# Optimization experiments

Hardware: AMD Instinct MI355X
Metric: run time of the kernel (lower is better)

The kernel has to match this reference:

```python
import jax, jax.numpy as jnp
import numpy as np

N_NODES = 20000
N_INPUT = 64
K_MAX = 12
BITS = 64
N_OUT = 10
BATCH = 64
T = 128


def setup_inputs() -> dict:
    key = jax.random.key(0)
    ks = jax.random.split(key, 8)
    x = jax.random.randint(ks[0], (BATCH, T, BITS), 0, 2, dtype=jnp.int32)
    w_in = jax.random.randint(ks[1], (BITS, N_INPUT), 0, 2, dtype=jnp.int32)
    adj_list = jax.random.randint(ks[2], (N_NODES, K_MAX), 0, N_NODES, dtype=jnp.int32)
    adj_mask = jax.random.randint(ks[3], (N_NODES, K_MAX), 0, 2, dtype=jnp.int32)
    lut = jax.random.randint(ks[4], (N_NODES, 2 ** K_MAX), 0, 2, dtype=jnp.int32)
    init_states = jax.random.randint(ks[5], (1, N_NODES), 0, 2, dtype=jnp.int32)
    W_out = jax.random.normal(ks[6], (N_OUT, N_NODES - N_INPUT), dtype=jnp.float32) * 0.02
    b_out = jnp.zeros((N_OUT,), dtype=jnp.float32)
    return {"x": x, "w_in": w_in, "adj_list": adj_list, "adj_mask": adj_mask,
            "lut": lut, "init_states": init_states, "W_out": W_out, "b_out": b_out}


def reference(x, w_in, adj_list, adj_mask, lut, init_states, W_out, b_out):
    B, T_, bits = x.shape
    N, k = adj_list.shape
    I = w_in.shape[1]
    # powers_of_2, big-endian order as in make_minimal_powers_of_two (flip)
    powers = (2 ** jnp.arange(k - 1, -1, -1)).astype(jnp.int32)  # [k]
    no_neigh = ~(adj_mask.astype(bool).any(axis=1))              # [N] nodes w/o neighbours keep state
    node_ids = jnp.arange(N)
    states0 = jnp.broadcast_to(init_states, (B, N)).astype(jnp.int32)

    def step(states, x_t):
        # inject input: bipartite mapping of input bits onto first I nodes (OR-combine)
        u = ((x_t @ w_in) > 0).astype(jnp.int32)                 # [B, I]
        states = states.at[:, :I].set(u)
        # gather incoming neighbour states per node (irregular gather)
        neigh = jnp.take(states, adj_list, axis=1)               # [B, N, k]
        neigh = neigh * adj_mask[None, :, :]
        # bit-pack into LUT index
        idx = (neigh * powers[None, None, :]).sum(axis=-1)       # [B, N], < 2^k
        new = lut[node_ids[None, :], idx]                        # [B, N] LUT lookup
        new = jnp.where(no_neigh[None, :], states, new)
        return new, None

    states, _ = jax.lax.scan(step, states0, jnp.swapaxes(x, 0, 1))
    # readout on reservoir (non-input) nodes at final timestep
    feats = states[:, I:].astype(jnp.float32)                    # [B, N-I]
    out = jax.nn.sigmoid(feats @ W_out.T + b_out)                # [B, n_outputs]
    return out
```

## Files before the change

kernel.cpp:

```cpp
#include <hip/hip_runtime.h>
#include <cstdint>
#include <cstddef>


#define N_NODES   20000
#define N_INPUT   64
#define K_MAX     12
#define T_STEPS   128
#define N_BATCH   64
#define N_OUT     10
#define N_FEAT    (N_NODES - N_INPUT)
#define DUMMY_NODE 20000
#define ST_WORDS  20004

#define NBLK 512
#define NTHR 512
#define NPB  39
#define NPB_PAD 40
#define BAR_CNT 64
#define GO_CNT  8
#define BAR_STRIDE 32

typedef unsigned long long u64;

__global__ __launch_bounds__(256) void pack_x_kernel(const int* __restrict__ x,
                                                     u64* __restrict__ xp) {
  const int t = blockIdx.x;
  const int wave = threadIdx.x >> 6, lane = threadIdx.x & 63;
  for (int b = wave; b < N_BATCH; b += 4) {
    int v = x[((size_t)b * T_STEPS + t) * 64 + lane];
    u64 bal = __ballot(v != 0);
    if (lane == 0) xp[(size_t)t * N_BATCH + b] = bal;
  }
}

__global__ __launch_bounds__(256) void init_kernel(const int* __restrict__ inis,
                                                   const int* __restrict__ w_in,
                                                   const u64* __restrict__ xp,
                                                   u64* __restrict__ buf0,
                                                   u64* __restrict__ buf1,
                                                   u64* __restrict__ wcol,
                                                   unsigned* __restrict__ bar) {
  if (blockIdx.x < 79) {
    int n = blockIdx.x * 256 + threadIdx.x;
    if (n >= N_INPUT && n < ST_WORDS) {
      u64 w = (n < N_NODES && inis[n] != 0) ? ~0ull : 0ull;
      buf0[n] = w;
      buf1[n] = w;
    }
  } else {
    const int wave = threadIdx.x >> 6, lane = threadIdx.x & 63;
    u64 xw = xp[lane];
    for (int i = wave; i < 64; i += 4) {
      int wv = w_in[(size_t)lane * 64 + i];
      u64 wc = __ballot(wv != 0);
      if (lane == 0) wcol[i] = wc;
      u64 ub = __ballot((xw & wc) != 0);
      if (lane == 0) buf0[i] = ub;
    }
    if (threadIdx.x < BAR_CNT + GO_CNT)
      bar[threadIdx.x * BAR_STRIDE] = 0u;
  }
}

__global__ __launch_bounds__(64) void u_pre_kernel(const u64* __restrict__ xp,
                                                   const u64* __restrict__ wcol,
                                                   u64* __restrict__ u_all) {
  const int t = blockIdx.x, lane = threadIdx.x;
  u64 xw = xp[(size_t)t * N_BATCH + lane];
  for (int i = 0; i < 64; i++) {
    u64 ub = __ballot((xw & wcol[i]) != 0);
    if (lane == 0) u_all[(size_t)t * 64 + i] = ub;
  }
}

__device__ __forceinline__ u64 bit_transpose64(u64 w, int lane) {
  const u64 LO0 = 0x00000000FFFFFFFFull, LO1 = 0x0000FFFF0000FFFFull,
            LO2 = 0x00FF00FF00FF00FFull, LO3 = 0x0F0F0F0F0F0F0F0Full,
            LO4 = 0x3333333333333333ull, LO5 = 0x5555555555555555ull;
#define XP_STAGE(d, LO)                                                  \
  {                                                                      \
    u64 p = (u64)__shfl_xor((long long)w, (d), 64);                      \
    if (lane & (d)) w = ((p >> (d)) & (LO)) | (w & ~(LO));               \
    else            w = (w & (LO)) | ((p << (d)) & ~(LO));               \
  }
  XP_STAGE(32, LO0) XP_STAGE(16, LO1) XP_STAGE(8, LO2)
  XP_STAGE(4,  LO3) XP_STAGE(2,  LO4) XP_STAGE(1, LO5)
#undef XP_STAGE
  return w;
}

__global__ __launch_bounds__(NTHR, 4) void reservoir_kernel(
    const int* __restrict__ lut, const int* __restrict__ adj,
    const int* __restrict__ mask, const u64* __restrict__ u_all,
    u64* __restrict__ buf0, u64* __restrict__ buf1,
    unsigned* __restrict__ bar) {
  __shared__ u64 lut_lds[NPB_PAD * 64];
  __shared__ int adj_lds[NPB_PAD * K_MAX];
  __shared__ unsigned char hn_lds[NPB_PAD];

  const int bi = blockIdx.x;
  const int tid = threadIdx.x;
  const int wave = tid >> 6, lane = tid & 63;
  const int base = N_INPUT + bi * NPB;
  const int nloc = min(NPB, N_NODES - base);

  if (tid < NPB_PAD) {
    int i = tid, h = 0;
    if (i < nloc) {
      for (int j = 0; j < K_MAX; j++) {
        int m = mask[(size_t)(base + i) * K_MAX + j];
        int a = adj[(size_t)(base + i) * K_MAX + j];
        adj_lds[i * K_MAX + (K_MAX - 1 - j)] = m ? a : DUMMY_NODE;
        h |= m;
      }
    } else {
      for (int j = 0; j < K_MAX; j++) adj_lds[i * K_MAX + j] = DUMMY_NODE;
    }
    hn_lds[i] = (unsigned char)(h ? 1 : 0);
  }

  const int nwords = nloc * 64;
  const int* lp = lut + (size_t)base * 4096;
  for (int w0 = wave * 8; w0 < nwords; w0 += 64) {
    int v[8];
#pragma unroll
    for (int q = 0; q < 8; q++) {
      int widx = w0 + q;
      v[q] = (widx < nwords) ? lp[(size_t)widx * 64 + lane] : 0;
    }
#pragma unroll
    for (int q = 0; q < 8; q++) {
      int widx = w0 + q;
      u64 bal = __ballot(v[q] != 0);
      if (lane == 0 && widx < nwords) lut_lds[widx] = bal;
    }
  }
  __syncthreads();

  const int l0 = wave * 5;
  const int cnt = min(5, nloc - l0);

  int my_a = DUMMY_NODE;
  if (lane < 60) my_a = adj_lds[l0 * K_MAX + lane];
  unsigned hmask = 0;
#pragma unroll
  for (int i = 0; i < 5; i++) hmask |= (unsigned)hn_lds[l0 + i] << i;

  for (int t = 0; t < T_STEPS; t++) {
    u64* cur = (t & 1) ? buf1 : buf0;
    u64* nxt = (t & 1) ? buf0 : buf1;

    u64 w = __hip_atomic_load(&cur[my_a], __ATOMIC_RELAXED,
                              __HIP_MEMORY_SCOPE_AGENT);
    w = bit_transpose64(w, lane);

#pragma unroll
    for (int i = 0; i < 5; i++) {
      if (i < cnt) {
        unsigned idx = (unsigned)(w >> (12 * i)) & 0xFFFu;
        u64 g = lut_lds[(l0 + i) * 64 + (idx >> 6)];
        u64 res = __ballot((g >> (idx & 63)) & 1ull);
        if (lane == 0 && ((hmask >> i) & 1u))
          __hip_atomic_store(&nxt[base + l0 + i], res,
                             __ATOMIC_RELAXED, __HIP_MEMORY_SCOPE_AGENT);
      }
    }

    if (bi == NBLK - 1 && wave == 7 && t + 1 < T_STEPS) {
      u64 uw = u_all[(size_t)(t + 1) * 64 + lane];
      __hip_atomic_store(&nxt[lane], uw, __ATOMIC_RELAXED, __HIP_MEMORY_SCOPE_AGENT);
    }

    if (t != T_STEPS - 1) {
      __syncthreads();
      __builtin_amdgcn_fence(__ATOMIC_RELEASE, "workgroup");
      if (tid == 0)
        __hip_atomic_fetch_add(&bar[(bi & (BAR_CNT - 1)) * BAR_STRIDE], 1u,
                               __ATOMIC_RELAXED, __HIP_MEMORY_SCOPE_AGENT);
      if (bi == 0 && wave == 0) {
        const unsigned tgt = (unsigned)(t + 1) * (NBLK / BAR_CNT);
        for (;;) {
          unsigned c = __hip_atomic_load(&bar[lane * BAR_STRIDE],
                                         __ATOMIC_RELAXED, __HIP_MEMORY_SCOPE_AGENT);
          if (__all(c >= tgt)) break;
        }
        if (lane < GO_CNT)
          __hip_atomic_store(&bar[(BAR_CNT + lane) * BAR_STRIDE], (unsigned)(t + 1),
                             __ATOMIC_RELAXED, __HIP_MEMORY_SCOPE_AGENT);
      } else if (wave == 0) {
        unsigned* gp = &bar[(BAR_CNT + (bi & (GO_CNT - 1))) * BAR_STRIDE];
        while (__hip_atomic_load(gp, __ATOMIC_RELAXED, __HIP_MEMORY_SCOPE_AGENT)
               < (unsigned)(t + 1)) {  }
      }
      __builtin_amdgcn_fence(__ATOMIC_ACQUIRE, "workgroup");
      __syncthreads();
    }
  }
}

__global__ __launch_bounds__(256) void readout_kernel(const u64* __restrict__ st,
                                                      const float* __restrict__ Wout,
                                                      const float* __restrict__ bout,
                                                      float* __restrict__ out) {
  const int b = blockIdx.x / N_OUT;
  const int o = blockIdx.x % N_OUT;
  float acc = 0.f;
  for (int n = threadIdx.x; n < N_FEAT; n += 256) {
    u64 s = st[N_INPUT + n];
    float w = Wout[(size_t)o * N_FEAT + n];
    acc += ((s >> b) & 1ull) ? w : 0.f;
  }
  for (int off = 32; off > 0; off >>= 1) acc += __shfl_down(acc, off);
  __shared__ float red[4];
  const int wave = threadIdx.x >> 6, lane = threadIdx.x & 63;
  if (lane == 0) red[wave] = acc;
  __syncthreads();
  if (threadIdx.x == 0) {
    float tot = red[0] + red[1] + red[2] + red[3] + bout[o];
    out[(size_t)b * N_OUT + o] = 1.f / (1.f + __expf(-tot));
  }
}

extern "C" void kernel_launch(void* const* d_in, const int* in_sizes, int n_in,
                              void* d_out, int out_size, void* d_ws, size_t ws_size,
                              hipStream_t stream) {
  const int* x    = (const int*)d_in[0];
  const int* w_in = (const int*)d_in[1];
  const int* adj  = (const int*)d_in[2];
  const int* mask = (const int*)d_in[3];
  const int* lut  = (const int*)d_in[4];
  const int* inis = (const int*)d_in[5];
  const float* Wout = (const float*)d_in[6];
  const float* bout = (const float*)d_in[7];
  float* out = (float*)d_out;

  char* ws = (char*)d_ws;
  size_t off = 0;
  auto alloc = [&](size_t bytes) -> void* {
    void* p = ws + off;
    off += (bytes + 255) & ~(size_t)255;
    return p;
  };
  u64* buf0 = (u64*)alloc((size_t)ST_WORDS * 8);
  u64* buf1 = (u64*)alloc((size_t)ST_WORDS * 8);
  u64* xp   = (u64*)alloc((size_t)T_STEPS * N_BATCH * 8);
  u64* wcol = (u64*)alloc(64 * 8);
  u64* u_all = (u64*)alloc((size_t)T_STEPS * 64 * 8);
  unsigned* bar = (unsigned*)alloc((size_t)(BAR_CNT + GO_CNT) * BAR_STRIDE * 4);
  (void)ws_size; (void)in_sizes; (void)n_in; (void)out_size;

  hipLaunchKernelGGL(pack_x_kernel, dim3(T_STEPS), dim3(256), 0, stream, x, xp);
  hipLaunchKernelGGL(init_kernel, dim3(80), dim3(256), 0, stream,
                     inis, w_in, xp, buf0, buf1, wcol, bar);
  hipLaunchKernelGGL(u_pre_kernel, dim3(T_STEPS), dim3(64), 0, stream,
                     xp, wcol, u_all);

  hipLaunchKernelGGL(reservoir_kernel, dim3(NBLK), dim3(NTHR), 0, stream,
                     lut, adj, mask, u_all, buf0, buf1, bar);

  hipLaunchKernelGGL(readout_kernel, dim3(N_BATCH * N_OUT), dim3(256), 0, stream,
                     buf0, Wout, bout, out);
}
```

Before: 963.8 us.

## Shrink persistent grid to 128 blocks, prepack LUT, flatten grid barrier

Reduces the persistent reservoir grid from 512 to 128 workgroups of 1024 threads, with each wave now handling 10 nodes through two gathers and transposes. This cuts the number of participants in the per-timestep grid barrier. The barrier drops the atomic fetch-add counters in favour of per-block flag stores, which block 0 scans with 64-bit loads, and the pollers keep a second load in flight. LUT bit-packing moves into a separate full-grid kernel, so the persistent kernel only copies pre-packed words into LDS. The trade-off is fewer blocks for latency hiding and an extra pass over the 328 MB LUT, though that pass is fully parallel.

```diff
diff --git a/kernel.cpp b/kernel.cpp
--- a/kernel.cpp
+++ b/kernel.cpp
@@ -13,13 +13,16 @@
 #define DUMMY_NODE 20000
 #define ST_WORDS  20004
 
-#define NBLK 512
-#define NTHR 512
-#define NPB  39
-#define NPB_PAD 40
-#define BAR_CNT 64
+#define NBLK 128
+#define NTHR 1024
+#define NWAVE 16
+#define NPW  10
+#define NPB  156
+#define NPB_PAD 160
+#define GO_OFF  256
 #define GO_CNT  8
-#define BAR_STRIDE 32
+#define GO_STRIDE 32
+#define PL_BLK 2500
 
 typedef unsigned long long u64;
 
@@ -31,6 +34,17 @@
     int v = x[((size_t)b * T_STEPS + t) * 64 + lane];
     u64 bal = __ballot(v != 0);
     if (lane == 0) xp[(size_t)t * N_BATCH + b] = bal;
+  }
+}
+
+__global__ __launch_bounds__(512) void pack_lut_kernel(const int* __restrict__ lut,
+                                                       u64* __restrict__ lutp) {
+  const int wave = threadIdx.x >> 6, lane = threadIdx.x & 63;
+  const int nwords = N_NODES * 64;
+  for (int widx = blockIdx.x * 8 + wave; widx < nwords; widx += PL_BLK * 8) {
+    int v = lut[(size_t)widx * 64 + lane];
+    u64 bal = __ballot(v != 0);
+    if (lane == 0) lutp[widx] = bal;
   }
 }
 
@@ -58,8 +72,10 @@
       u64 ub = __ballot((xw & wc) != 0);
       if (lane == 0) buf0[i] = ub;
     }
-    if (threadIdx.x < BAR_CNT + GO_CNT)
-      bar[threadIdx.x * BAR_STRIDE] = 0u;
+    if (threadIdx.x < NBLK)
+      bar[threadIdx.x] = 0u;
+    else if (threadIdx.x < NBLK + GO_CNT)
+      bar[GO_OFF + (threadIdx.x - NBLK) * GO_STRIDE] = 0u;
   }
 }
 
@@ -91,7 +107,7 @@
 }
 
 __global__ __launch_bounds__(NTHR, 4) void reservoir_kernel(
-    const int* __restrict__ lut, const int* __restrict__ adj,
+    const u64* __restrict__ lutp, const int* __restrict__ adj,
     const int* __restrict__ mask, const u64* __restrict__ u_all,
     u64* __restrict__ buf0, u64* __restrict__ buf1,
     unsigned* __restrict__ bar) {
@@ -120,45 +136,37 @@
     hn_lds[i] = (unsigned char)(h ? 1 : 0);
   }
 
+  const u64* lp = lutp + (size_t)base * 64;
   const int nwords = nloc * 64;
-  const int* lp = lut + (size_t)base * 4096;
-  for (int w0 = wave * 8; w0 < nwords; w0 += 64) {
-    int v[8];
-#pragma unroll
-    for (int q = 0; q < 8; q++) {
-      int widx = w0 + q;
-      v[q] = (widx < nwords) ? lp[(size_t)widx * 64 + lane] : 0;
-    }
-#pragma unroll
-    for (int q = 0; q < 8; q++) {
-      int widx = w0 + q;
-      u64 bal = __ballot(v[q] != 0);
-      if (lane == 0 && widx < nwords) lut_lds[widx] = bal;
-    }
-  }
+  for (int idx = tid; idx < nwords; idx += NTHR)
+    lut_lds[idx] = lp[idx];
   __syncthreads();
 
-  const int l0 = wave * 5;
-  const int cnt = min(5, nloc - l0);
-
-  int my_a = DUMMY_NODE;
-  if (lane < 60) my_a = adj_lds[l0 * K_MAX + lane];
+  const int l0 = wave * NPW;
+  const int cnt = min(NPW, nloc - l0);
+
+  int a0 = DUMMY_NODE, a1 = DUMMY_NODE;
+  if (lane < 60) {
+    a0 = adj_lds[l0 * K_MAX + lane];
+    a1 = adj_lds[(l0 + 5) * K_MAX + lane];
+  }
   unsigned hmask = 0;
 #pragma unroll
-  for (int i = 0; i < 5; i++) hmask |= (unsigned)hn_lds[l0 + i] << i;
+  for (int i = 0; i < NPW; i++) hmask |= (unsigned)hn_lds[l0 + i] << i;
 
   for (int t = 0; t < T_STEPS; t++) {
     u64* cur = (t & 1) ? buf1 : buf0;
     u64* nxt = (t & 1) ? buf0 : buf1;
 
-    u64 w = __hip_atomic_load(&cur[my_a], __ATOMIC_RELAXED,
-                              __HIP_MEMORY_SCOPE_AGENT);
-    w = bit_transpose64(w, lane);
+    u64 w0 = __hip_atomic_load(&cur[a0], __ATOMIC_RELAXED, __HIP_MEMORY_SCOPE_AGENT);
+    u64 w1 = __hip_atomic_load(&cur[a1], __ATOMIC_RELAXED, __HIP_MEMORY_SCOPE_AGENT);
+    w0 = bit_transpose64(w0, lane);
+    w1 = bit_transpose64(w1, lane);
 
 #pragma unroll
     for (int i = 0; i < 5; i++) {
       if (i < cnt) {
-        unsigned idx = (unsigned)(w >> (12 * i)) & 0xFFFu;
+        unsigned idx = (unsigned)(w0 >> (12 * i)) & 0xFFFu;
         u64 g = lut_lds[(l0 + i) * 64 + (idx >> 6)];
         u64 res = __ballot((g >> (idx & 63)) & 1ull);
         if (lane == 0 && ((hmask >> i) & 1u))
@@ -166,32 +174,50 @@
                              __ATOMIC_RELAXED, __HIP_MEMORY_SCOPE_AGENT);
       }
     }
-
-    if (bi == NBLK - 1 && wave == 7 && t + 1 < T_STEPS) {
+#pragma unroll
+    for (int i = 0; i < 5; i++) {
+      if (i + 5 < cnt) {
+        unsigned idx = (unsigned)(w1 >> (12 * i)) & 0xFFFu;
+        u64 g = lut_lds[(l0 + 5 + i) * 64 + (idx >> 6)];
+        u64 res = __ballot((g >> (idx & 63)) & 1ull);
+        if (lane == 0 && ((hmask >> (i + 5)) & 1u))
+          __hip_atomic_store(&nxt[base + l0 + 5 + i], res,
+                             __ATOMIC_RELAXED, __HIP_MEMORY_SCOPE_AGENT);
+      }
+    }
+
+    if (bi == NBLK - 1 && wave == NWAVE - 1 && t + 1 < T_STEPS) {
       u64 uw = u_all[(size_t)(t + 1) * 64 + lane];
       __hip_atomic_store(&nxt[lane], uw, __ATOMIC_RELAXED, __HIP_MEMORY_SCOPE_AGENT);
     }
 
     if (t != T_STEPS - 1) {
+      const unsigned tgt = (unsigned)(t + 1);
       __syncthreads();
       __builtin_amdgcn_fence(__ATOMIC_RELEASE, "workgroup");
       if (tid == 0)
-        __hip_atomic_fetch_add(&bar[(bi & (BAR_CNT - 1)) * BAR_STRIDE], 1u,
-                               __ATOMIC_RELAXED, __HIP_MEMORY_SCOPE_AGENT);
+        __hip_atomic_store(&bar[bi], tgt, __ATOMIC_RELAXED, __HIP_MEMORY_SCOPE_AGENT);
       if (bi == 0 && wave == 0) {
-        const unsigned tgt = (unsigned)(t + 1) * (NBLK / BAR_CNT);
+        const u64* fp = (const u64*)bar;
+        u64 fa = __hip_atomic_load(&fp[lane], __ATOMIC_RELAXED, __HIP_MEMORY_SCOPE_AGENT);
+        u64 fb = __hip_atomic_load(&fp[lane], __ATOMIC_RELAXED, __HIP_MEMORY_SCOPE_AGENT);
         for (;;) {
-          unsigned c = __hip_atomic_load(&bar[lane * BAR_STRIDE],
-                                         __ATOMIC_RELAXED, __HIP_MEMORY_SCOPE_AGENT);
-          if (__all(c >= tgt)) break;
+          bool ok = ((unsigned)fa >= tgt) && ((unsigned)(fa >> 32) >= tgt);
+          if (__all(ok)) break;
+          fa = fb;
+          fb = __hip_atomic_load(&fp[lane], __ATOMIC_RELAXED, __HIP_MEMORY_SCOPE_AGENT);
         }
         if (lane < GO_CNT)
-          __hip_atomic_store(&bar[(BAR_CNT + lane) * BAR_STRIDE], (unsigned)(t + 1),
+          __hip_atomic_store(&bar[GO_OFF + lane * GO_STRIDE], tgt,
                              __ATOMIC_RELAXED, __HIP_MEMORY_SCOPE_AGENT);
       } else if (wave == 0) {
-        unsigned* gp = &bar[(BAR_CNT + (bi & (GO_CNT - 1))) * BAR_STRIDE];
-        while (__hip_atomic_load(gp, __ATOMIC_RELAXED, __HIP_MEMORY_SCOPE_AGENT)
-               < (unsigned)(t + 1)) {  }
+        unsigned* gp = &bar[GO_OFF + (bi & (GO_CNT - 1)) * GO_STRIDE];
+        unsigned ga = __hip_atomic_load(gp, __ATOMIC_RELAXED, __HIP_MEMORY_SCOPE_AGENT);
+        unsigned gb = __hip_atomic_load(gp, __ATOMIC_RELAXED, __HIP_MEMORY_SCOPE_AGENT);
+        while (ga < tgt) {
+          ga = gb;
+          gb = __hip_atomic_load(gp, __ATOMIC_RELAXED, __HIP_MEMORY_SCOPE_AGENT);
+        }
       }
       __builtin_amdgcn_fence(__ATOMIC_ACQUIRE, "workgroup");
       __syncthreads();
@@ -247,17 +273,19 @@
   u64* xp   = (u64*)alloc((size_t)T_STEPS * N_BATCH * 8);
   u64* wcol = (u64*)alloc(64 * 8);
   u64* u_all = (u64*)alloc((size_t)T_STEPS * 64 * 8);
-  unsigned* bar = (unsigned*)alloc((size_t)(BAR_CNT + GO_CNT) * BAR_STRIDE * 4);
+  unsigned* bar = (unsigned*)alloc((size_t)(GO_OFF + GO_CNT * GO_STRIDE) * 4);
+  u64* lutp = (u64*)alloc((size_t)N_NODES * 64 * 8);
   (void)ws_size; (void)in_sizes; (void)n_in; (void)out_size;
 
   hipLaunchKernelGGL(pack_x_kernel, dim3(T_STEPS), dim3(256), 0, stream, x, xp);
+  hipLaunchKernelGGL(pack_lut_kernel, dim3(PL_BLK), dim3(512), 0, stream, lut, lutp);
   hipLaunchKernelGGL(init_kernel, dim3(80), dim3(256), 0, stream,
                      inis, w_in, xp, buf0, buf1, wcol, bar);
   hipLaunchKernelGGL(u_pre_kernel, dim3(T_STEPS), dim3(64), 0, stream,
                      xp, wcol, u_all);
 
   hipLaunchKernelGGL(reservoir_kernel, dim3(NBLK), dim3(NTHR), 0, stream,
-                     lut, adj, mask, u_all, buf0, buf1, bar);
+                     lutp, adj, mask, u_all, buf0, buf1, bar);
 
   hipLaunchKernelGGL(readout_kernel, dim3(N_BATCH * N_OUT), dim3(256), 0, stream,
                      buf0, Wout, bout, out);
```

Measured after the change: 1.097 ms. +13.8%, slower.

## Replace centralized grid barrier with per-step state buffers and flag polling

Applied to the files above, without the earlier changes.

Keeps a separate state buffer for every timestep, so writes never race with reads of older states. The centralized counter-and-go barrier is replaced by per-block step flags, replicated four ways, which one watcher wave per block polls before releasing the other waves through LDS. Input injection is precomputed straight into each step's buffer, and LUT bit-packing moves into a separate grid-wide pre-kernel instead of running inside each persistent block. The cost is a larger workspace (129 state copies plus the packed LUT), filling every buffer with the initial state, and spin-waiting on LDS.

```diff
diff --git a/kernel.cpp b/kernel.cpp
--- a/kernel.cpp
+++ b/kernel.cpp
@@ -12,14 +12,18 @@
 #define N_FEAT    (N_NODES - N_INPUT)
 #define DUMMY_NODE 20000
 #define ST_WORDS  20004
+#define T_BUF     (T_STEPS + 1)
 
 #define NBLK 512
 #define NTHR 512
 #define NPB  39
 #define NPB_PAD 40
-#define BAR_CNT 64
-#define GO_CNT  8
-#define BAR_STRIDE 32
+#define WATCH_WAVE 7
+#define FL_REP 4
+#define FL_STRIDE 1024
+#define PL_FILL 39
+#define PL_LUT  2500
+#define PL_TOT  (PL_FILL + PL_LUT)
 
 typedef unsigned long long u64;
 
@@ -34,43 +38,52 @@
   }
 }
 
-__global__ __launch_bounds__(256) void init_kernel(const int* __restrict__ inis,
-                                                   const int* __restrict__ w_in,
-                                                   const u64* __restrict__ xp,
-                                                   u64* __restrict__ buf0,
-                                                   u64* __restrict__ buf1,
-                                                   u64* __restrict__ wcol,
-                                                   unsigned* __restrict__ bar) {
-  if (blockIdx.x < 79) {
-    int n = blockIdx.x * 256 + threadIdx.x;
-    if (n >= N_INPUT && n < ST_WORDS) {
+__global__ __launch_bounds__(512) void pack_lut_fill_kernel(
+    const int* __restrict__ lut, const int* __restrict__ inis,
+    u64* __restrict__ lutp, u64* __restrict__ st_all) {
+  if (blockIdx.x < PL_FILL) {
+    int n = N_INPUT + blockIdx.x * 512 + threadIdx.x;
+    if (n < ST_WORDS) {
       u64 w = (n < N_NODES && inis[n] != 0) ? ~0ull : 0ull;
-      buf0[n] = w;
-      buf1[n] = w;
+      for (int t = 0; t < T_BUF; t++)
+        st_all[(size_t)t * ST_WORDS + n] = w;
     }
   } else {
     const int wave = threadIdx.x >> 6, lane = threadIdx.x & 63;
-    u64 xw = xp[lane];
+    const int nwords = N_NODES * 64;
+    for (int widx = (blockIdx.x - PL_FILL) * 8 + wave; widx < nwords;
+         widx += PL_LUT * 8) {
+      int v = lut[(size_t)widx * 64 + lane];
+      u64 bal = __ballot(v != 0);
+      if (lane == 0) lutp[widx] = bal;
+    }
+  }
+}
+
+__global__ __launch_bounds__(256) void init_kernel(const int* __restrict__ w_in,
+                                                   u64* __restrict__ wcol,
+                                                   unsigned* __restrict__ fl) {
+  if (blockIdx.x == 0) {
+    const int wave = threadIdx.x >> 6, lane = threadIdx.x & 63;
     for (int i = wave; i < 64; i += 4) {
       int wv = w_in[(size_t)lane * 64 + i];
       u64 wc = __ballot(wv != 0);
       if (lane == 0) wcol[i] = wc;
-      u64 ub = __ballot((xw & wc) != 0);
-      if (lane == 0) buf0[i] = ub;
-    }
-    if (threadIdx.x < BAR_CNT + GO_CNT)
-      bar[threadIdx.x * BAR_STRIDE] = 0u;
+    }
+  } else {
+    for (int k = threadIdx.x; k < FL_REP * FL_STRIDE; k += 256)
+      fl[k] = 0u;
   }
 }
 
 __global__ __launch_bounds__(64) void u_pre_kernel(const u64* __restrict__ xp,
                                                    const u64* __restrict__ wcol,
-                                                   u64* __restrict__ u_all) {
+                                                   u64* __restrict__ st_all) {
   const int t = blockIdx.x, lane = threadIdx.x;
   u64 xw = xp[(size_t)t * N_BATCH + lane];
   for (int i = 0; i < 64; i++) {
     u64 ub = __ballot((xw & wcol[i]) != 0);
-    if (lane == 0) u_all[(size_t)t * 64 + i] = ub;
+    if (lane == 0) st_all[(size_t)t * ST_WORDS + i] = ub;
   }
 }
 
@@ -91,19 +104,21 @@
 }
 
 __global__ __launch_bounds__(NTHR, 4) void reservoir_kernel(
-    const int* __restrict__ lut, const int* __restrict__ adj,
-    const int* __restrict__ mask, const u64* __restrict__ u_all,
-    u64* __restrict__ buf0, u64* __restrict__ buf1,
-    unsigned* __restrict__ bar) {
+    const u64* __restrict__ lutp, const int* __restrict__ adj,
+    const int* __restrict__ mask, u64* __restrict__ st_all,
+    unsigned* __restrict__ fl) {
   __shared__ u64 lut_lds[NPB_PAD * 64];
   __shared__ int adj_lds[NPB_PAD * K_MAX];
   __shared__ unsigned char hn_lds[NPB_PAD];
+  __shared__ int avail_lds;
 
   const int bi = blockIdx.x;
   const int tid = threadIdx.x;
   const int wave = tid >> 6, lane = tid & 63;
   const int base = N_INPUT + bi * NPB;
   const int nloc = min(NPB, N_NODES - base);
+
+  if (tid == 0) avail_lds = 0;
 
   if (tid < NPB_PAD) {
     int i = tid, h = 0;
@@ -120,39 +135,51 @@
     hn_lds[i] = (unsigned char)(h ? 1 : 0);
   }
 
+  const u64* lp = lutp + (size_t)base * 64;
   const int nwords = nloc * 64;
-  const int* lp = lut + (size_t)base * 4096;
-  for (int w0 = wave * 8; w0 < nwords; w0 += 64) {
-    int v[8];
-#pragma unroll
-    for (int q = 0; q < 8; q++) {
-      int widx = w0 + q;
-      v[q] = (widx < nwords) ? lp[(size_t)widx * 64 + lane] : 0;
-    }
-#pragma unroll
-    for (int q = 0; q < 8; q++) {
-      int widx = w0 + q;
-      u64 bal = __ballot(v[q] != 0);
-      if (lane == 0 && widx < nwords) lut_lds[widx] = bal;
-    }
-  }
+  for (int idx = tid; idx < nwords; idx += NTHR)
+    lut_lds[idx] = lp[idx];
   __syncthreads();
 
   const int l0 = wave * 5;
   const int cnt = min(5, nloc - l0);
 
-  int my_a = DUMMY_NODE;
-  if (lane < 60) my_a = adj_lds[l0 * K_MAX + lane];
+  int a0 = DUMMY_NODE;
+  if (lane < 60) a0 = adj_lds[l0 * K_MAX + lane];
   unsigned hmask = 0;
 #pragma unroll
   for (int i = 0; i < 5; i++) hmask |= (unsigned)hn_lds[l0 + i] << i;
 
+  const u64* fp = (const u64*)(fl + (size_t)(bi & (FL_REP - 1)) * FL_STRIDE);
+
   for (int t = 0; t < T_STEPS; t++) {
-    u64* cur = (t & 1) ? buf1 : buf0;
-    u64* nxt = (t & 1) ? buf0 : buf1;
-
-    u64 w = __hip_atomic_load(&cur[my_a], __ATOMIC_RELAXED,
-                              __HIP_MEMORY_SCOPE_AGENT);
+    if (t) {
+      if (wave == WATCH_WAVE) {
+        const unsigned tgt = (unsigned)t;
+        for (;;) {
+          u64 f0 = __hip_atomic_load(&fp[lane],       __ATOMIC_RELAXED, __HIP_MEMORY_SCOPE_AGENT);
+          u64 f1 = __hip_atomic_load(&fp[64 + lane],  __ATOMIC_RELAXED, __HIP_MEMORY_SCOPE_AGENT);
+          u64 f2 = __hip_atomic_load(&fp[128 + lane], __ATOMIC_RELAXED, __HIP_MEMORY_SCOPE_AGENT);
+          u64 f3 = __hip_atomic_load(&fp[192 + lane], __ATOMIC_RELAXED, __HIP_MEMORY_SCOPE_AGENT);
+          bool ok = (unsigned)f0 >= tgt && (unsigned)(f0 >> 32) >= tgt &&
+                    (unsigned)f1 >= tgt && (unsigned)(f1 >> 32) >= tgt &&
+                    (unsigned)f2 >= tgt && (unsigned)(f2 >> 32) >= tgt &&
+                    (unsigned)f3 >= tgt && (unsigned)(f3 >> 32) >= tgt;
+          if (__all(ok)) break;
+        }
+        __builtin_amdgcn_fence(__ATOMIC_ACQUIRE, "workgroup");
+        if (lane == 0)
+          __hip_atomic_store(&avail_lds, t, __ATOMIC_RELAXED, __HIP_MEMORY_SCOPE_WORKGROUP);
+      } else {
+        while (__hip_atomic_load(&avail_lds, __ATOMIC_RELAXED, __HIP_MEMORY_SCOPE_WORKGROUP) < t) {}
+        __builtin_amdgcn_fence(__ATOMIC_ACQUIRE, "workgroup");
+      }
+    }
+
+    const u64* stc = st_all + (size_t)t * ST_WORDS;
+    u64* stn = st_all + (size_t)(t + 1) * ST_WORDS;
+
+    u64 w = __hip_atomic_load(&stc[a0], __ATOMIC_RELAXED, __HIP_MEMORY_SCOPE_AGENT);
     w = bit_transpose64(w, lane);
 
 #pragma unroll
@@ -162,39 +189,17 @@
         u64 g = lut_lds[(l0 + i) * 64 + (idx >> 6)];
         u64 res = __ballot((g >> (idx & 63)) & 1ull);
         if (lane == 0 && ((hmask >> i) & 1u))
-          __hip_atomic_store(&nxt[base + l0 + i], res,
+          __hip_atomic_store(&stn[base + l0 + i], res,
                              __ATOMIC_RELAXED, __HIP_MEMORY_SCOPE_AGENT);
       }
-    }
-
-    if (bi == NBLK - 1 && wave == 7 && t + 1 < T_STEPS) {
-      u64 uw = u_all[(size_t)(t + 1) * 64 + lane];
-      __hip_atomic_store(&nxt[lane], uw, __ATOMIC_RELAXED, __HIP_MEMORY_SCOPE_AGENT);
     }
 
     if (t != T_STEPS - 1) {
       __syncthreads();
       __builtin_amdgcn_fence(__ATOMIC_RELEASE, "workgroup");
-      if (tid == 0)
-        __hip_atomic_fetch_add(&bar[(bi & (BAR_CNT - 1)) * BAR_STRIDE], 1u,
-                               __ATOMIC_RELAXED, __HIP_MEMORY_SCOPE_AGENT);
-      if (bi == 0 && wave == 0) {
-        const unsigned tgt = (unsigned)(t + 1) * (NBLK / BAR_CNT);
-        for (;;) {
-          unsigned c = __hip_atomic_load(&bar[lane * BAR_STRIDE],
-                                         __ATOMIC_RELAXED, __HIP_MEMORY_SCOPE_AGENT);
-          if (__all(c >= tgt)) break;
-        }
-        if (lane < GO_CNT)
-          __hip_atomic_store(&bar[(BAR_CNT + lane) * BAR_STRIDE], (unsigned)(t + 1),
-                             __ATOMIC_RELAXED, __HIP_MEMORY_SCOPE_AGENT);
-      } else if (wave == 0) {
-        unsigned* gp = &bar[(BAR_CNT + (bi & (GO_CNT - 1))) * BAR_STRIDE];
-        while (__hip_atomic_load(gp, __ATOMIC_RELAXED, __HIP_MEMORY_SCOPE_AGENT)
-               < (unsigned)(t + 1)) {  }
-      }
-      __builtin_amdgcn_fence(__ATOMIC_ACQUIRE, "workgroup");
-      __syncthreads();
+      if (tid < FL_REP)
+        __hip_atomic_store(&fl[tid * FL_STRIDE + bi], (unsigned)(t + 1),
+                           __ATOMIC_RELAXED, __HIP_MEMORY_SCOPE_AGENT);
     }
   }
 }
@@ -242,23 +247,23 @@
     off += (bytes + 255) & ~(size_t)255;
     return p;
   };
-  u64* buf0 = (u64*)alloc((size_t)ST_WORDS * 8);
-  u64* buf1 = (u64*)alloc((size_t)ST_WORDS * 8);
-  u64* xp   = (u64*)alloc((size_t)T_STEPS * N_BATCH * 8);
-  u64* wcol = (u64*)alloc(64 * 8);
-  u64* u_all = (u64*)alloc((size_t)T_STEPS * 64 * 8);
-  unsigned* bar = (unsigned*)alloc((size_t)(BAR_CNT + GO_CNT) * BAR_STRIDE * 4);
+  u64* st_all = (u64*)alloc((size_t)T_BUF * ST_WORDS * 8);
+  u64* xp     = (u64*)alloc((size_t)T_STEPS * N_BATCH * 8);
+  u64* wcol   = (u64*)alloc(64 * 8);
+  unsigned* fl = (unsigned*)alloc((size_t)FL_REP * FL_STRIDE * 4);
+  u64* lutp   = (u64*)alloc((size_t)N_NODES * 64 * 8);
   (void)ws_size; (void)in_sizes; (void)n_in; (void)out_size;
 
   hipLaunchKernelGGL(pack_x_kernel, dim3(T_STEPS), dim3(256), 0, stream, x, xp);
-  hipLaunchKernelGGL(init_kernel, dim3(80), dim3(256), 0, stream,
-                     inis, w_in, xp, buf0, buf1, wcol, bar);
+  hipLaunchKernelGGL(pack_lut_fill_kernel, dim3(PL_TOT), dim3(512), 0, stream,
+                     lut, inis, lutp, st_all);
+  hipLaunchKernelGGL(init_kernel, dim3(2), dim3(256), 0, stream, w_in, wcol, fl);
   hipLaunchKernelGGL(u_pre_kernel, dim3(T_STEPS), dim3(64), 0, stream,
-                     xp, wcol, u_all);
+                     xp, wcol, st_all);
 
   hipLaunchKernelGGL(reservoir_kernel, dim3(NBLK), dim3(NTHR), 0, stream,
-                     lut, adj, mask, u_all, buf0, buf1, bar);
+                     lutp, adj, mask, st_all, fl);
 
   hipLaunchKernelGGL(readout_kernel, dim3(N_BATCH * N_OUT), dim3(256), 0, stream,
-                     buf0, Wout, bout, out);
-}
+                     st_all + (size_t)T_STEPS * ST_WORDS, Wout, bout, out);
+}
```

Result: slower. 1.208 ms (+25.4%).

## Replace atomic-counter grid barrier with per-block flags and split readout

Applied to the files above, without the earlier changes.

The grid barrier no longer has blocks fetch-add into 64 shared counters. Each block now stores the step number into its own flag word, and block 0 polls all 512 flags with packed 64-bit loads before releasing the go flags. This is meant to remove atomic RMW contention on the barrier counters at every timestep. The readout also changes: each thread now handles one batch bit across a chunk of features, partial sums go to a buffer, and a second tiny kernel reduces them and applies the sigmoid. The aim is to cut redundant reads of the state and W_out, at the cost of one extra kernel launch.

```diff
diff --git a/kernel.cpp b/kernel.cpp
--- a/kernel.cpp
+++ b/kernel.cpp
@@ -17,9 +17,13 @@
 #define NTHR 512
 #define NPB  39
 #define NPB_PAD 40
-#define BAR_CNT 64
+#define GO_OFF  512
 #define GO_CNT  8
-#define BAR_STRIDE 32
+#define GO_STRIDE 32
+#define FL_TOT  (GO_OFF + GO_CNT * GO_STRIDE)
+
+#define RO_CHUNK 32
+#define RO_NPC   623
 
 typedef unsigned long long u64;
 
@@ -40,7 +44,7 @@
                                                    u64* __restrict__ buf0,
                                                    u64* __restrict__ buf1,
                                                    u64* __restrict__ wcol,
-                                                   unsigned* __restrict__ bar) {
+                                                   unsigned* __restrict__ fl) {
   if (blockIdx.x < 79) {
     int n = blockIdx.x * 256 + threadIdx.x;
     if (n >= N_INPUT && n < ST_WORDS) {
@@ -58,8 +62,8 @@
       u64 ub = __ballot((xw & wc) != 0);
       if (lane == 0) buf0[i] = ub;
     }
-    if (threadIdx.x < BAR_CNT + GO_CNT)
-      bar[threadIdx.x * BAR_STRIDE] = 0u;
+    for (int k = threadIdx.x; k < FL_TOT; k += 256)
+      fl[k] = 0u;
   }
 }
 
@@ -94,7 +98,7 @@
     const int* __restrict__ lut, const int* __restrict__ adj,
     const int* __restrict__ mask, const u64* __restrict__ u_all,
     u64* __restrict__ buf0, u64* __restrict__ buf1,
-    unsigned* __restrict__ bar) {
+    unsigned* __restrict__ fl) {
   __shared__ u64 lut_lds[NPB_PAD * 64];
   __shared__ int adj_lds[NPB_PAD * K_MAX];
   __shared__ unsigned char hn_lds[NPB_PAD];
@@ -141,8 +145,8 @@
   const int l0 = wave * 5;
   const int cnt = min(5, nloc - l0);
 
-  int my_a = DUMMY_NODE;
-  if (lane < 60) my_a = adj_lds[l0 * K_MAX + lane];
+  int a0 = DUMMY_NODE;
+  if (lane < 60) a0 = adj_lds[l0 * K_MAX + lane];
   unsigned hmask = 0;
 #pragma unroll
   for (int i = 0; i < 5; i++) hmask |= (unsigned)hn_lds[l0 + i] << i;
@@ -151,8 +155,7 @@
     u64* cur = (t & 1) ? buf1 : buf0;
     u64* nxt = (t & 1) ? buf0 : buf1;
 
-    u64 w = __hip_atomic_load(&cur[my_a], __ATOMIC_RELAXED,
-                              __HIP_MEMORY_SCOPE_AGENT);
+    u64 w = __hip_atomic_load(&cur[a0], __ATOMIC_RELAXED, __HIP_MEMORY_SCOPE_AGENT);
     w = bit_transpose64(w, lane);
 
 #pragma unroll
@@ -173,25 +176,29 @@
     }
 
     if (t != T_STEPS - 1) {
+      const unsigned tgt = (unsigned)(t + 1);
       __syncthreads();
       __builtin_amdgcn_fence(__ATOMIC_RELEASE, "workgroup");
       if (tid == 0)
-        __hip_atomic_fetch_add(&bar[(bi & (BAR_CNT - 1)) * BAR_STRIDE], 1u,
-                               __ATOMIC_RELAXED, __HIP_MEMORY_SCOPE_AGENT);
+        __hip_atomic_store(&fl[bi], tgt, __ATOMIC_RELAXED, __HIP_MEMORY_SCOPE_AGENT);
       if (bi == 0 && wave == 0) {
-        const unsigned tgt = (unsigned)(t + 1) * (NBLK / BAR_CNT);
+        const u64* fp = (const u64*)fl;
+        const u64 want = ((u64)tgt << 32) | (u64)tgt;
         for (;;) {
-          unsigned c = __hip_atomic_load(&bar[lane * BAR_STRIDE],
-                                         __ATOMIC_RELAXED, __HIP_MEMORY_SCOPE_AGENT);
-          if (__all(c >= tgt)) break;
+          u64 f0 = __hip_atomic_load(&fp[lane],       __ATOMIC_RELAXED, __HIP_MEMORY_SCOPE_AGENT);
+          u64 f1 = __hip_atomic_load(&fp[64 + lane],  __ATOMIC_RELAXED, __HIP_MEMORY_SCOPE_AGENT);
+          u64 f2 = __hip_atomic_load(&fp[128 + lane], __ATOMIC_RELAXED, __HIP_MEMORY_SCOPE_AGENT);
+          u64 f3 = __hip_atomic_load(&fp[192 + lane], __ATOMIC_RELAXED, __HIP_MEMORY_SCOPE_AGENT);
+          bool ok = (f0 == want) && (f1 == want) && (f2 == want) && (f3 == want);
+          if (__all(ok)) break;
         }
         if (lane < GO_CNT)
-          __hip_atomic_store(&bar[(BAR_CNT + lane) * BAR_STRIDE], (unsigned)(t + 1),
+          __hip_atomic_store(&fl[GO_OFF + lane * GO_STRIDE], tgt,
                              __ATOMIC_RELAXED, __HIP_MEMORY_SCOPE_AGENT);
       } else if (wave == 0) {
-        unsigned* gp = &bar[(BAR_CNT + (bi & (GO_CNT - 1))) * BAR_STRIDE];
+        unsigned* gp = &fl[GO_OFF + (bi & (GO_CNT - 1)) * GO_STRIDE];
         while (__hip_atomic_load(gp, __ATOMIC_RELAXED, __HIP_MEMORY_SCOPE_AGENT)
-               < (unsigned)(t + 1)) {  }
+               < tgt) {  }
       }
       __builtin_amdgcn_fence(__ATOMIC_ACQUIRE, "workgroup");
       __syncthreads();
@@ -199,27 +206,36 @@
   }
 }
 
-__global__ __launch_bounds__(256) void readout_kernel(const u64* __restrict__ st,
-                                                      const float* __restrict__ Wout,
-                                                      const float* __restrict__ bout,
-                                                      float* __restrict__ out) {
-  const int b = blockIdx.x / N_OUT;
+__global__ __launch_bounds__(256) void readout_part(const u64* __restrict__ st,
+                                                    const float* __restrict__ Wout,
+                                                    float* __restrict__ partial) {
+  const int c = blockIdx.x / N_OUT;
   const int o = blockIdx.x % N_OUT;
+  const int b = threadIdx.x & 63, k = threadIdx.x >> 6;
+  const int n0 = c * RO_NPC, n1 = n0 + RO_NPC;
   float acc = 0.f;
-  for (int n = threadIdx.x; n < N_FEAT; n += 256) {
+  for (int n = n0 + k; n < n1; n += 4) {
     u64 s = st[N_INPUT + n];
     float w = Wout[(size_t)o * N_FEAT + n];
     acc += ((s >> b) & 1ull) ? w : 0.f;
   }
-  for (int off = 32; off > 0; off >>= 1) acc += __shfl_down(acc, off);
-  __shared__ float red[4];
-  const int wave = threadIdx.x >> 6, lane = threadIdx.x & 63;
-  if (lane == 0) red[wave] = acc;
+  __shared__ float red[4][64];
+  red[k][b] = acc;
   __syncthreads();
-  if (threadIdx.x == 0) {
-    float tot = red[0] + red[1] + red[2] + red[3] + bout[o];
-    out[(size_t)b * N_OUT + o] = 1.f / (1.f + __expf(-tot));
-  }
+  if (threadIdx.x < 64) {
+    float tot = red[0][b] + red[1][b] + red[2][b] + red[3][b];
+    partial[((size_t)c * N_OUT + o) * 64 + b] = tot;
+  }
+}
+
+__global__ __launch_bounds__(640) void readout_final(const float* __restrict__ partial,
+                                                     const float* __restrict__ bout,
+                                                     float* __restrict__ out) {
+  const int b = threadIdx.x & 63, o = threadIdx.x >> 6;
+  float tot = bout[o];
+  for (int c = 0; c < RO_CHUNK; c++)
+    tot += partial[((size_t)c * N_OUT + o) * 64 + b];
+  out[(size_t)b * N_OUT + o] = 1.f / (1.f + __expf(-tot));
 }
 
 extern "C" void kernel_launch(void* const* d_in, const int* in_sizes, int n_in,
@@ -247,18 +263,21 @@
   u64* xp   = (u64*)alloc((size_t)T_STEPS * N_BATCH * 8);
   u64* wcol = (u64*)alloc(64 * 8);
   u64* u_all = (u64*)alloc((size_t)T_STEPS * 64 * 8);
-  unsigned* bar = (unsigned*)alloc((size_t)(BAR_CNT + GO_CNT) * BAR_STRIDE * 4);
+  unsigned* fl = (unsigned*)alloc((size_t)FL_TOT * 4);
+  float* partial = (float*)alloc((size_t)RO_CHUNK * N_OUT * 64 * 4);
   (void)ws_size; (void)in_sizes; (void)n_in; (void)out_size;
 
   hipLaunchKernelGGL(pack_x_kernel, dim3(T_STEPS), dim3(256), 0, stream, x, xp);
   hipLaunchKernelGGL(init_kernel, dim3(80), dim3(256), 0, stream,
-                     inis, w_in, xp, buf0, buf1, wcol, bar);
+                     inis, w_in, xp, buf0, buf1, wcol, fl);
   hipLaunchKernelGGL(u_pre_kernel, dim3(T_STEPS), dim3(64), 0, stream,
                      xp, wcol, u_all);
 
   hipLaunchKernelGGL(reservoir_kernel, dim3(NBLK), dim3(NTHR), 0, stream,
-                     lut, adj, mask, u_all, buf0, buf1, bar);
-
-  hipLaunchKernelGGL(readout_kernel, dim3(N_BATCH * N_OUT), dim3(256), 0, stream,
-                     buf0, Wout, bout, out);
-}
+                     lut, adj, mask, u_all, buf0, buf1, fl);
+
+  hipLaunchKernelGGL(readout_part, dim3(RO_CHUNK * N_OUT), dim3(256), 0, stream,
+                     buf0, Wout, partial);
+  hipLaunchKernelGGL(readout_final, dim3(1), dim3(640), 0, stream,
+                     partial, bout, out);
+}
```

Result: slower. 1.004 ms (+4.2%).
